# Optimization experiments

Hardware: AMD Instinct MI355X
Metric: run time of the kernel (lower is better)

## Reference

```python
import jax, jax.numpy as jnp
import numpy as np

EMB = 8
HID = 64
B = 1000
T = 512
N = (B * T) // 5  # events per source; sources partition the (batch,time) grid

_KEYS = ["ccba", "cdtx", "cust", "dp", "remit"]
_NUMS = {"ccba": 8, "cdtx": 1, "cust": 1, "dp": 2, "remit": 1}
_CATS = {"ccba": 0, "cdtx": 2, "cust": 3, "dp": 8, "remit": 1}
_VOCAB = {"ccba": 0, "cdtx": 179, "cust": 37, "dp": 435, "remit": 5}


def setup_inputs() -> dict:
    ks = iter(jax.random.split(jax.random.key(0), 64))
    rng = np.random.default_rng(0)
    chunks = np.split(rng.permutation(B * T), 5)
    d = {}
    for k5, ch in zip(_KEYS, chunks):
        d[k5 + "_num"] = jax.random.normal(next(ks), (N, _NUMS[k5]), jnp.float32)
        if _CATS[k5] > 0:
            d[k5 + "_cat"] = jax.random.randint(next(ks), (N, _CATS[k5]), 0, _VOCAB[k5])
            d[k5 + "_tab"] = jax.random.normal(next(ks), (_VOCAB[k5], EMB), jnp.float32) * 0.1
        d[k5 + "_bi"] = jnp.asarray(ch // T, jnp.int32)
        d[k5 + "_ti"] = jnp.asarray(ch % T, jnp.int32)
        in_dim = _CATS[k5] * EMB + _NUMS[k5]
        d[k5 + "_W"] = jax.random.normal(next(ks), (in_dim, HID), jnp.float32) * np.float32(1.0 / np.sqrt(in_dim))
        d[k5 + "_b"] = jnp.zeros((HID,), jnp.float32)
    # LSTM: 2 layers x 2 directions, hidden 64, proj_size 1 -> layer1 input is 2
    for l, insz in [(0, HID), (1, 2)]:
        d[f"Wih{l}"] = jax.random.normal(next(ks), (2, 4 * HID, insz), jnp.float32) * 0.05
        d[f"Whh{l}"] = jax.random.normal(next(ks), (2, 4 * HID, 1), jnp.float32) * 0.05
        d[f"Whr{l}"] = jax.random.normal(next(ks), (2, 1, HID), jnp.float32) * 0.05
        d[f"bih{l}"] = jnp.zeros((2, 4 * HID), jnp.float32)
        d[f"bhh{l}"] = jnp.zeros((2, 4 * HID), jnp.float32)
    d["length"] = T
    d["batch_size"] = B
    return d


def _embed(num, cat, tab, W, b):
    # FeatureEmbedder: concat(categorical embeddings, numeric) -> Linear(hidden)
    x = num if cat is None else jnp.concatenate([tab[cat].reshape(cat.shape[0], -1), num], axis=-1)
    return x @ W + b


def _lstm_dir(x, Wih, Whh, Whr, bih, bhh, reverse):
    Bx = x.shape[0]
    H = Whr.shape[1]
    p = Whr.shape[0]
    bias = bih + bhh

    def step(carry, xt):
        h, c = carry  # h: [B,p] projected hidden, c: [B,H] cell
        g = xt @ Wih.T + h @ Whh.T + bias
        i, f, gg, o = jnp.split(g, 4, axis=-1)  # PyTorch gate order i,f,g,o
        c = jax.nn.sigmoid(f) * c + jax.nn.sigmoid(i) * jnp.tanh(gg)
        h = (jax.nn.sigmoid(o) * jnp.tanh(c)) @ Whr.T  # proj_size projection
        return (h, c), h

    init = (jnp.zeros((Bx, p), x.dtype), jnp.zeros((Bx, H), x.dtype))
    _, ys = jax.lax.scan(step, init, jnp.swapaxes(x, 0, 1), reverse=reverse)
    return jnp.swapaxes(ys, 0, 1)  # [B,T,p]


def _bilstm(x, Wih, Whh, Whr, bih, bhh):
    fwd = _lstm_dir(x, Wih[0], Whh[0], Whr[0], bih[0], bhh[0], False)
    bwd = _lstm_dir(x, Wih[1], Whh[1], Whr[1], bih[1], bhh[1], True)
    return jnp.concatenate([fwd, bwd], axis=-1)


def _forward(a):
    feat = jnp.zeros((a["batch_size"], a["length"], HID), jnp.float32)
    for k5 in _KEYS:
        v = _embed(a[k5 + "_num"], a.get(k5 + "_cat"), a.get(k5 + "_tab"), a[k5 + "_W"], a[k5 + "_b"])
        feat = feat.at[a[k5 + "_bi"], a[k5 + "_ti"]].set(v)  # scatter-assemble padded tensor
    h = _bilstm(feat, a["Wih0"], a["Whh0"], a["Whr0"], a["bih0"], a["bhh0"])
    h = _bilstm(h, a["Wih1"], a["Whh1"], a["Whr1"], a["bih1"], a["bhh1"])
    return h.mean(axis=2)  # [B,T]


def reference(ccba_num, ccba_bi, ccba_ti, ccba_W, ccba_b,
              cdtx_num, cdtx_cat, cdtx_tab, cdtx_bi, cdtx_ti, cdtx_W, cdtx_b,
              cust_num, cust_cat, cust_tab, cust_bi, cust_ti, cust_W, cust_b,
              dp_num, dp_cat, dp_tab, dp_bi, dp_ti, dp_W, dp_b,
              remit_num, remit_cat, remit_tab, remit_bi, remit_ti, remit_W, remit_b,
              Wih0, Whh0, Whr0, bih0, bhh0, Wih1, Whh1, Whr1, bih1, bhh1,
              length, batch_size):
    return _forward(dict(locals()))
```

## Files before the change

### kernel.cpp

```cpp
#include <hip/hip_runtime.h>
#include <cstdint>
#include <cstddef>

#define TLEN 512
#define BATCH 1000
#define NEVS 102400
#define HID 64

__device__ __forceinline__ float fast_rcp(float x) {
#if __has_builtin(__builtin_amdgcn_rcpf)
    return __builtin_amdgcn_rcpf(x);
#else
    return 1.0f / x;
#endif
}
__device__ __forceinline__ float sigm(float x) { return fast_rcp(1.0f + __expf(-x)); }
__device__ __forceinline__ float tanh_f(float x) { return fmaf(2.0f, sigm(2.0f * x), -1.0f); }

__device__ __forceinline__ float wave_sum_bcast(float x) {
#if __has_builtin(__builtin_amdgcn_update_dpp) && __has_builtin(__builtin_amdgcn_readlane)
    x += __int_as_float(__builtin_amdgcn_update_dpp(0, __float_as_int(x), 0x111, 0xf, 0xf, true));
    x += __int_as_float(__builtin_amdgcn_update_dpp(0, __float_as_int(x), 0x112, 0xf, 0xf, true));
    x += __int_as_float(__builtin_amdgcn_update_dpp(0, __float_as_int(x), 0x114, 0xf, 0xf, true));
    x += __int_as_float(__builtin_amdgcn_update_dpp(0, __float_as_int(x), 0x118, 0xf, 0xf, true));
    x += __int_as_float(__builtin_amdgcn_update_dpp(0, __float_as_int(x), 0x142, 0xa, 0xf, true));
    x += __int_as_float(__builtin_amdgcn_update_dpp(0, __float_as_int(x), 0x143, 0xc, 0xf, true));
    return __int_as_float(__builtin_amdgcn_readlane(__float_as_int(x), 63));
#else
#pragma unroll
    for (int off = 1; off < 64; off <<= 1) x += __shfl_xor(x, off, 64);
    return x;
#endif
}

__global__ __launch_bounds__(512) void compose_kernel(
    const float* __restrict__ W0, const float* __restrict__ B0,
    const float* __restrict__ W1, const float* __restrict__ B1,
    const float* __restrict__ W2, const float* __restrict__ B2,
    const float* __restrict__ W3, const float* __restrict__ B3,
    const float* __restrict__ W4, const float* __restrict__ B4,
    const float* __restrict__ Wih, const float* __restrict__ bih,
    const float* __restrict__ bhh, float* __restrict__ wp)
{
    const int col = threadIdx.x;
    const int row = blockIdx.x;
    const float* srcW; const float* srcB; int base, IND;
    if (row < 9)        { srcW = W0; srcB = B0; base = 0;   IND = 8;  }
    else if (row < 27)  { srcW = W1; srcB = B1; base = 9;   IND = 17; }
    else if (row < 53)  { srcW = W2; srcB = B2; base = 27;  IND = 25; }
    else if (row < 120) { srcW = W3; srcB = B3; base = 53;  IND = 66; }
    else                { srcW = W4; srcB = B4; base = 120; IND = 9;  }
    const int j = row - base;
    const float* xrow = (j < IND) ? (srcW + (size_t)j * 64) : srcB;
    const float* wr = Wih + (size_t)col * 64;
    float acc = 0.0f;
#pragma unroll
    for (int h2 = 0; h2 < 64; ++h2) acc = fmaf(xrow[h2], wr[h2], acc);
    if (j == IND) acc += bih[col] + bhh[col];
    wp[(size_t)row * 512 + col] = acc;
}

template<int NNUM, int NCAT>
__device__ __forceinline__ void project_src(
    const float* __restrict__ num, const int* __restrict__ cat,
    const float* __restrict__ tab, const int* __restrict__ bi,
    const int* __restrict__ ti, const float* __restrict__ wrows,
    float* __restrict__ gdst, int dir, int lo, int hi, int tcm,
    int* qcnt, int* queue)
{
    constexpr int IND = NCAT * 8 + NNUM;
    const int tid = threadIdx.x;
    const int col = dir * 256 + tid;
    float wcol[IND];
#pragma unroll
    for (int j = 0; j < IND; ++j) wcol[j] = wrows[(size_t)j * 512 + col];
    const float bcol = wrows[(size_t)IND * 512 + col];

    const int S = gridDim.x;
    const int per = (NEVS + S - 1) / S;
    const int e0 = blockIdx.x * per;
    const int e1 = (e0 + per < NEVS) ? (e0 + per) : NEVS;

    for (int base = e0; base < e1; base += 256) {
        if (tid == 0) *qcnt = 0;
        __syncthreads();
        {
            const int ev = base + tid;
            if (ev < e1) {
                const int t = ti[ev];
                if (t >= lo && t < hi) {
                    const int s = atomicAdd(qcnt, 1);
                    queue[s] = ev;
                }
            }
        }
        __syncthreads();
        const int n = *qcnt;
        for (int i = 0; i < n; i += 2) {
            const int eA = __builtin_amdgcn_readfirstlane(queue[i]);
            const bool two = (i + 1 < n);
            const int eB = two ? __builtin_amdgcn_readfirstlane(queue[i + 1]) : eA;
            float accA = bcol, accB = bcol;
#pragma unroll
            for (int c0 = 0; c0 < NCAT; ++c0) {
                const int ia = cat[eA * NCAT + c0];
                const int ib = cat[eB * NCAT + c0];
                const float* ta = tab + (size_t)ia * 8;
                const float* tb = tab + (size_t)ib * 8;
#pragma unroll
                for (int u = 0; u < 8; ++u) {
                    accA = fmaf(ta[u], wcol[c0 * 8 + u], accA);
                    accB = fmaf(tb[u], wcol[c0 * 8 + u], accB);
                }
            }
#pragma unroll
            for (int u = 0; u < NNUM; ++u) {
                accA = fmaf(num[(size_t)eA * NNUM + u], wcol[NCAT * 8 + u], accA);
                accB = fmaf(num[(size_t)eB * NNUM + u], wcol[NCAT * 8 + u], accB);
            }
            {
                const int tA = ti[eA], pA = bi[eA];
                const int lA = dir ? (hi - 1 - tA) : (tA - lo);
                gdst[((size_t)pA * tcm + lA) * 256 + tid] = accA;
            }
            if (two) {
                const int tB = ti[eB], pB = bi[eB];
                const int lB = dir ? (hi - 1 - tB) : (tB - lo);
                gdst[((size_t)pB * tcm + lB) * 256 + tid] = accB;
            }
        }
        __syncthreads();
    }
}

__global__ __launch_bounds__(256) void project_chunk_kernel(
    const float* __restrict__ ccba_num, const int* __restrict__ ccba_bi, const int* __restrict__ ccba_ti,
    const float* __restrict__ cdtx_num, const int* __restrict__ cdtx_cat, const float* __restrict__ cdtx_tab,
    const int* __restrict__ cdtx_bi, const int* __restrict__ cdtx_ti,
    const float* __restrict__ cust_num, const int* __restrict__ cust_cat, const float* __restrict__ cust_tab,
    const int* __restrict__ cust_bi, const int* __restrict__ cust_ti,
    const float* __restrict__ dp_num, const int* __restrict__ dp_cat, const float* __restrict__ dp_tab,
    const int* __restrict__ dp_bi, const int* __restrict__ dp_ti,
    const float* __restrict__ remit_num, const int* __restrict__ remit_cat, const float* __restrict__ remit_tab,
    const int* __restrict__ remit_bi, const int* __restrict__ remit_ti,
    const float* __restrict__ wp, float* __restrict__ gf, float* __restrict__ gb,
    int f0, int len, int tcm)
{
    __shared__ int qcnt;
    __shared__ int queue[256];
    const int dir = blockIdx.y & 1;
    const int src = blockIdx.y >> 1;
    const int lo = dir ? (TLEN - f0 - len) : f0;
    const int hi = lo + len;
    float* gdst = dir ? gb : gf;
    switch (src) {
        case 0: project_src<8, 0>(ccba_num, nullptr, nullptr, ccba_bi, ccba_ti, wp + 0 * 512,   gdst, dir, lo, hi, tcm, &qcnt, queue); break;
        case 1: project_src<1, 2>(cdtx_num, cdtx_cat, cdtx_tab, cdtx_bi, cdtx_ti, wp + 9 * 512,  gdst, dir, lo, hi, tcm, &qcnt, queue); break;
        case 2: project_src<1, 3>(cust_num, cust_cat, cust_tab, cust_bi, cust_ti, wp + 27 * 512, gdst, dir, lo, hi, tcm, &qcnt, queue); break;
        case 3: project_src<2, 8>(dp_num,   dp_cat,   dp_tab,   dp_bi,   dp_ti,   wp + 53 * 512, gdst, dir, lo, hi, tcm, &qcnt, queue); break;
        default: project_src<1, 1>(remit_num, remit_cat, remit_tab, remit_bi, remit_ti, wp + 120 * 512, gdst, dir, lo, hi, tcm, &qcnt, queue); break;
    }
}

__global__ __launch_bounds__(256) void rec_chunk_kernel(
    const float* __restrict__ gf, const float* __restrict__ gb,
    const float* __restrict__ Whh, const float* __restrict__ Whr,
    float* __restrict__ h0, float* __restrict__ hs, float* __restrict__ cs,
    int f0, int len, int tcm, int first)
{
    const int wv = threadIdx.x >> 6, lane = threadIdx.x & 63;
    const int p = blockIdx.x * 4 + wv;
    const int b = p >> 1, dir = p & 1;

    float whh4[4];
#pragma unroll
    for (int k = 0; k < 4; ++k) whh4[k] = Whh[dir * 256 + k * 64 + lane];
    const float whr = Whr[dir * HID + lane];

    const float* g = (dir ? gb : gf) + (size_t)b * tcm * 256 + lane;
    float* h0p = h0 + (size_t)b * TLEN * 2 + dir;

    float h, c;
    if (first) { h = 0.0f; c = 0.0f; }
    else       { h = hs[p]; c = cs[(size_t)p * 64 + lane]; }

    float A[4];
#pragma unroll
    for (int k = 0; k < 4; ++k) A[k] = g[k * 64];

    for (int s = 0; s < len; ++s) {
        float Nx[4];
        const int sn = (s + 1 < len) ? (s + 1) : s;
        const float* gn = g + (size_t)sn * 256;
#pragma unroll
        for (int k = 0; k < 4; ++k) Nx[k] = gn[k * 64];

        const float gi = fmaf(whh4[0], h, A[0]);
        const float gfv = fmaf(whh4[1], h, A[1]);
        const float gg = fmaf(whh4[2], h, A[2]);
        const float go = fmaf(whh4[3], h, A[3]);
        c = sigm(gfv) * c + sigm(gi) * tanh_f(gg);
        h = wave_sum_bcast(sigm(go) * tanh_f(c) * whr);
        const int t_out = dir ? (TLEN - 1 - f0 - s) : (f0 + s);
        if (lane == 0) h0p[(size_t)t_out * 2] = h;
#pragma unroll
        for (int k = 0; k < 4; ++k) A[k] = Nx[k];
    }
    if (lane == 0) hs[p] = h;
    cs[(size_t)p * 64 + lane] = c;
}

__global__ __launch_bounds__(256) void lstm1_kernel(
    const float* __restrict__ h0, const float* __restrict__ Wih,
    const float* __restrict__ Whh, const float* __restrict__ Whr,
    const float* __restrict__ bih, const float* __restrict__ bhh,
    float* __restrict__ h1)
{
    int w = threadIdx.x >> 6, lane = threadIdx.x & 63;
    int p = blockIdx.x * 4 + w;
    int b = p >> 1, dir = p & 1;

    float wi0[4], wi1[4], whh[4], bias[4];
#pragma unroll
    for (int k = 0; k < 4; ++k) {
        int r = k * 64 + lane;
        wi0[k] = Wih[(size_t)(dir * 256 + r) * 2 + 0];
        wi1[k] = Wih[(size_t)(dir * 256 + r) * 2 + 1];
        whh[k] = Whh[dir * 256 + r];
        bias[k] = bih[dir * 256 + r] + bhh[dir * 256 + r];
    }
    float whr = Whr[dir * HID + lane];
    float h = 0.0f, c = 0.0f;
    const float* hb = h0 + (size_t)b * TLEN * 2;

    auto xat = [&](int t) -> float2 {
        int tc = t < TLEN ? t : TLEN - 1;
        int tt = dir ? (TLEN - 1 - tc) : tc;
        return *(const float2*)(hb + (size_t)tt * 2);
    };

    float2 xA = xat(0), xB = xat(1);
    for (int t = 0; t < TLEN; t += 2) {
        float2 xC = xat(t + 2), xD = xat(t + 3);
        {
            float g[4];
#pragma unroll
            for (int k = 0; k < 4; ++k)
                g[k] = fmaf(whh[k], h, fmaf(wi1[k], xA.y, fmaf(wi0[k], xA.x, bias[k])));
            c = sigm(g[1]) * c + sigm(g[0]) * tanh_f(g[2]);
            h = wave_sum_bcast(sigm(g[3]) * tanh_f(c) * whr);
            int tt = dir ? (TLEN - 1 - t) : t;
            if (lane == 0) h1[((size_t)b * TLEN + tt) * 2 + dir] = h;
        }
        {
            float g[4];
#pragma unroll
            for (int k = 0; k < 4; ++k)
                g[k] = fmaf(whh[k], h, fmaf(wi1[k], xB.y, fmaf(wi0[k], xB.x, bias[k])));
            c = sigm(g[1]) * c + sigm(g[0]) * tanh_f(g[2]);
            h = wave_sum_bcast(sigm(g[3]) * tanh_f(c) * whr);
            int tt = dir ? (TLEN - 2 - t) : (t + 1);
            if (lane == 0) h1[((size_t)b * TLEN + tt) * 2 + dir] = h;
        }
        xA = xC; xB = xD;
    }
}

__global__ __launch_bounds__(256) void mean_kernel(
    const float2* __restrict__ h1, float* __restrict__ out)
{
    int i = blockIdx.x * 256 + threadIdx.x;
    if (i < BATCH * TLEN) {
        float2 v = h1[i];
        out[i] = 0.5f * (v.x + v.y);
    }
}

extern "C" void kernel_launch(void* const* d_in, const int* in_sizes, int n_in,
                              void* d_out, int out_size, void* d_ws, size_t ws_size,
                              hipStream_t stream)
{
    const float* ccba_num = (const float*)d_in[0];
    const int*   ccba_bi  = (const int*)d_in[1];
    const int*   ccba_ti  = (const int*)d_in[2];
    const float* ccba_W   = (const float*)d_in[3];
    const float* ccba_b   = (const float*)d_in[4];
    const float* cdtx_num = (const float*)d_in[5];
    const int*   cdtx_cat = (const int*)d_in[6];
    const float* cdtx_tab = (const float*)d_in[7];
    const int*   cdtx_bi  = (const int*)d_in[8];
    const int*   cdtx_ti  = (const int*)d_in[9];
    const float* cdtx_W   = (const float*)d_in[10];
    const float* cdtx_b   = (const float*)d_in[11];
    const float* cust_num = (const float*)d_in[12];
    const int*   cust_cat = (const int*)d_in[13];
    const float* cust_tab = (const float*)d_in[14];
    const int*   cust_bi  = (const int*)d_in[15];
    const int*   cust_ti  = (const int*)d_in[16];
    const float* cust_W   = (const float*)d_in[17];
    const float* cust_b   = (const float*)d_in[18];
    const float* dp_num   = (const float*)d_in[19];
    const int*   dp_cat   = (const int*)d_in[20];
    const float* dp_tab   = (const float*)d_in[21];
    const int*   dp_bi    = (const int*)d_in[22];
    const int*   dp_ti    = (const int*)d_in[23];
    const float* dp_W     = (const float*)d_in[24];
    const float* dp_b     = (const float*)d_in[25];
    const float* remit_num = (const float*)d_in[26];
    const int*   remit_cat = (const int*)d_in[27];
    const float* remit_tab = (const float*)d_in[28];
    const int*   remit_bi  = (const int*)d_in[29];
    const int*   remit_ti  = (const int*)d_in[30];
    const float* remit_W   = (const float*)d_in[31];
    const float* remit_b   = (const float*)d_in[32];
    const float* Wih0 = (const float*)d_in[33];
    const float* Whh0 = (const float*)d_in[34];
    const float* Whr0 = (const float*)d_in[35];
    const float* bih0 = (const float*)d_in[36];
    const float* bhh0 = (const float*)d_in[37];
    const float* Wih1 = (const float*)d_in[38];
    const float* Whh1 = (const float*)d_in[39];
    const float* Whr1 = (const float*)d_in[40];
    const float* bih1 = (const float*)d_in[41];
    const float* bhh1 = (const float*)d_in[42];

    float* out = (float*)d_out;

    const size_t FIXED = 4096000ull + 4096000ull + 266240ull + 8000ull + 512000ull;
    size_t avail = (ws_size > FIXED) ? (ws_size - FIXED) : 0;
    int tcm = (int)(avail / 2048000ull);
    if (tcm < 1) tcm = 1;
    if (tcm > TLEN) tcm = TLEN;

    char* ws = (char*)d_ws;
    const size_t gfB = (size_t)tcm * 1024000ull;
    float* gf = (float*)ws;
    float* gb = (float*)(ws + gfB);
    float* h0 = (float*)(ws + 2 * gfB);
    float* h1 = (float*)(ws + 2 * gfB + 4096000ull);
    float* wp = (float*)(ws + 2 * gfB + 8192000ull);
    float* hs = (float*)(ws + 2 * gfB + 8192000ull + 266240ull);
    float* cs = (float*)(ws + 2 * gfB + 8192000ull + 266240ull + 8000ull);

    compose_kernel<<<130, 512, 0, stream>>>(
        ccba_W, ccba_b, cdtx_W, cdtx_b, cust_W, cust_b,
        dp_W, dp_b, remit_W, remit_b, Wih0, bih0, bhh0, wp);

    int first = 1;
    for (int f0 = 0; f0 < TLEN; f0 += tcm) {
        const int len = (TLEN - f0 < tcm) ? (TLEN - f0) : tcm;
        project_chunk_kernel<<<dim3(256, 10), 256, 0, stream>>>(
            ccba_num, ccba_bi, ccba_ti,
            cdtx_num, cdtx_cat, cdtx_tab, cdtx_bi, cdtx_ti,
            cust_num, cust_cat, cust_tab, cust_bi, cust_ti,
            dp_num, dp_cat, dp_tab, dp_bi, dp_ti,
            remit_num, remit_cat, remit_tab, remit_bi, remit_ti,
            wp, gf, gb, f0, len, tcm);
        rec_chunk_kernel<<<500, 256, 0, stream>>>(
            gf, gb, Whh0, Whr0, h0, hs, cs, f0, len, tcm, first);
        first = 0;
    }

    lstm1_kernel<<<500, 256, 0, stream>>>(h0, Wih1, Whh1, Whr1, bih1, bhh1, h1);
    mean_kernel<<<(BATCH * TLEN + 255) / 256, 256, 0, stream>>>((const float2*)h1, out);
}
```

Measured before the change: 1.471 ms.

## Bin events by time with counting sort to avoid rescanning all events per chunk

Adds a counting-sort preprocessing pass (count, scan, scatter) that groups each source's events by time index. The chunked projection kernel can then walk only the events in its time range instead of filtering every event in every chunk through a shared-memory queue. The projection now handles four events per iteration, runs with a doubled grid, and the recurrence loop prefetches two steps ahead. It also caps the chunk length at 86 and forces it even, which can add chunk launches, and the extra binning kernels and workspace add fixed overhead.

```diff
diff --git a/kernel.cpp b/kernel.cpp
--- a/kernel.cpp
+++ b/kernel.cpp
@@ -31,6 +31,55 @@
     for (int off = 1; off < 64; off <<= 1) x += __shfl_xor(x, off, 64);
     return x;
 #endif
+}
+
+__global__ __launch_bounds__(256) void bin_zero_kernel(int* __restrict__ cnt)
+{
+    int i = blockIdx.x * 256 + threadIdx.x;
+    if (i < 5 * 512) cnt[i] = 0;
+}
+
+__global__ __launch_bounds__(256) void bin_count_kernel(
+    const int* __restrict__ t0, const int* __restrict__ t1,
+    const int* __restrict__ t2, const int* __restrict__ t3,
+    const int* __restrict__ t4, int* __restrict__ cnt)
+{
+    const int src = blockIdx.y;
+    const int* ti = src == 0 ? t0 : src == 1 ? t1 : src == 2 ? t2 : src == 3 ? t3 : t4;
+    const int e = blockIdx.x * 256 + threadIdx.x;
+    atomicAdd(&cnt[src * 512 + ti[e]], 1);
+}
+
+__global__ __launch_bounds__(512) void bin_scan_kernel(
+    const int* __restrict__ cnt, int* __restrict__ startp, int* __restrict__ cur)
+{
+    const int src = blockIdx.x, tid = threadIdx.x;
+    __shared__ int s[512];
+    const int v = cnt[src * 512 + tid];
+    s[tid] = v;
+    __syncthreads();
+    for (int off = 1; off < 512; off <<= 1) {
+        int t = (tid >= off) ? s[tid - off] : 0;
+        __syncthreads();
+        s[tid] += t;
+        __syncthreads();
+    }
+    const int inc = s[tid];
+    startp[src * 513 + tid] = inc - v;
+    cur[src * 512 + tid] = inc - v;
+    if (tid == 511) startp[src * 513 + 512] = inc;
+}
+
+__global__ __launch_bounds__(256) void bin_scatter_kernel(
+    const int* __restrict__ t0, const int* __restrict__ t1,
+    const int* __restrict__ t2, const int* __restrict__ t3,
+    const int* __restrict__ t4, int* __restrict__ cur, int* __restrict__ order)
+{
+    const int src = blockIdx.y;
+    const int* ti = src == 0 ? t0 : src == 1 ? t1 : src == 2 ? t2 : src == 3 ? t3 : t4;
+    const int e = blockIdx.x * 256 + threadIdx.x;
+    const int off = atomicAdd(&cur[src * 512 + ti[e]], 1);
+    order[(size_t)src * NEVS + off] = e;
 }
 
 __global__ __launch_bounds__(512) void compose_kernel(
@@ -65,8 +114,8 @@
     const float* __restrict__ num, const int* __restrict__ cat,
     const float* __restrict__ tab, const int* __restrict__ bi,
     const int* __restrict__ ti, const float* __restrict__ wrows,
-    float* __restrict__ gdst, int dir, int lo, int hi, int tcm,
-    int* qcnt, int* queue)
+    const int* __restrict__ order_s, const int* __restrict__ start_s,
+    float* __restrict__ gdst, int dir, int lo, int hi, int tcm)
 {
     constexpr int IND = NCAT * 8 + NNUM;
     const int tid = threadIdx.x;
@@ -76,60 +125,50 @@
     for (int j = 0; j < IND; ++j) wcol[j] = wrows[(size_t)j * 512 + col];
     const float bcol = wrows[(size_t)IND * 512 + col];
 
-    const int S = gridDim.x;
-    const int per = (NEVS + S - 1) / S;
-    const int e0 = blockIdx.x * per;
-    const int e1 = (e0 + per < NEVS) ? (e0 + per) : NEVS;
-
-    for (int base = e0; base < e1; base += 256) {
-        if (tid == 0) *qcnt = 0;
-        __syncthreads();
-        {
-            const int ev = base + tid;
-            if (ev < e1) {
-                const int t = ti[ev];
-                if (t >= lo && t < hi) {
-                    const int s = atomicAdd(qcnt, 1);
-                    queue[s] = ev;
-                }
+    const int r0 = start_s[lo];
+    const int r1 = start_s[hi];
+
+    for (int i = r0 + (int)blockIdx.x * 4; i < r1; i += (int)gridDim.x * 4) {
+        int ebuf[4], tE[4], pE[4];
+#pragma unroll
+        for (int k = 0; k < 4; ++k) {
+            const int j = i + k;
+            ebuf[k] = __builtin_amdgcn_readfirstlane(order_s[(j < r1) ? j : i]);
+        }
+#pragma unroll
+        for (int k = 0; k < 4; ++k) { tE[k] = ti[ebuf[k]]; pE[k] = bi[ebuf[k]]; }
+
+        float acc[4] = {bcol, bcol, bcol, bcol};
+#pragma unroll
+        for (int c0 = 0; c0 < NCAT; ++c0) {
+            const float* t0 = tab + (size_t)cat[ebuf[0] * NCAT + c0] * 8;
+            const float* t1 = tab + (size_t)cat[ebuf[1] * NCAT + c0] * 8;
+            const float* t2 = tab + (size_t)cat[ebuf[2] * NCAT + c0] * 8;
+            const float* t3 = tab + (size_t)cat[ebuf[3] * NCAT + c0] * 8;
+#pragma unroll
+            for (int u = 0; u < 8; ++u) {
+                const float w = wcol[c0 * 8 + u];
+                acc[0] = fmaf(t0[u], w, acc[0]);
+                acc[1] = fmaf(t1[u], w, acc[1]);
+                acc[2] = fmaf(t2[u], w, acc[2]);
+                acc[3] = fmaf(t3[u], w, acc[3]);
             }
         }
-        __syncthreads();
-        const int n = *qcnt;
-        for (int i = 0; i < n; i += 2) {
-            const int eA = __builtin_amdgcn_readfirstlane(queue[i]);
-            const bool two = (i + 1 < n);
-            const int eB = two ? __builtin_amdgcn_readfirstlane(queue[i + 1]) : eA;
-            float accA = bcol, accB = bcol;
-#pragma unroll
-            for (int c0 = 0; c0 < NCAT; ++c0) {
-                const int ia = cat[eA * NCAT + c0];
-                const int ib = cat[eB * NCAT + c0];
-                const float* ta = tab + (size_t)ia * 8;
-                const float* tb = tab + (size_t)ib * 8;
-#pragma unroll
-                for (int u = 0; u < 8; ++u) {
-                    accA = fmaf(ta[u], wcol[c0 * 8 + u], accA);
-                    accB = fmaf(tb[u], wcol[c0 * 8 + u], accB);
-                }
+#pragma unroll
+        for (int u = 0; u < NNUM; ++u) {
+            const float w = wcol[NCAT * 8 + u];
+            acc[0] = fmaf(num[(size_t)ebuf[0] * NNUM + u], w, acc[0]);
+            acc[1] = fmaf(num[(size_t)ebuf[1] * NNUM + u], w, acc[1]);
+            acc[2] = fmaf(num[(size_t)ebuf[2] * NNUM + u], w, acc[2]);
+            acc[3] = fmaf(num[(size_t)ebuf[3] * NNUM + u], w, acc[3]);
+        }
+#pragma unroll
+        for (int k = 0; k < 4; ++k) {
+            if (i + k < r1) {
+                const int l = dir ? (hi - 1 - tE[k]) : (tE[k] - lo);
+                gdst[((size_t)pE[k] * tcm + l) * 256 + tid] = acc[k];
             }
-#pragma unroll
-            for (int u = 0; u < NNUM; ++u) {
-                accA = fmaf(num[(size_t)eA * NNUM + u], wcol[NCAT * 8 + u], accA);
-                accB = fmaf(num[(size_t)eB * NNUM + u], wcol[NCAT * 8 + u], accB);
-            }
-            {
-                const int tA = ti[eA], pA = bi[eA];
-                const int lA = dir ? (hi - 1 - tA) : (tA - lo);
-                gdst[((size_t)pA * tcm + lA) * 256 + tid] = accA;
-            }
-            if (two) {
-                const int tB = ti[eB], pB = bi[eB];
-                const int lB = dir ? (hi - 1 - tB) : (tB - lo);
-                gdst[((size_t)pB * tcm + lB) * 256 + tid] = accB;
-            }
-        }
-        __syncthreads();
+        }
     }
 }
 
@@ -143,22 +182,23 @@
     const int* __restrict__ dp_bi, const int* __restrict__ dp_ti,
     const float* __restrict__ remit_num, const int* __restrict__ remit_cat, const float* __restrict__ remit_tab,
     const int* __restrict__ remit_bi, const int* __restrict__ remit_ti,
-    const float* __restrict__ wp, float* __restrict__ gf, float* __restrict__ gb,
+    const float* __restrict__ wp, const int* __restrict__ order, const int* __restrict__ startp,
+    float* __restrict__ gf, float* __restrict__ gb,
     int f0, int len, int tcm)
 {
-    __shared__ int qcnt;
-    __shared__ int queue[256];
     const int dir = blockIdx.y & 1;
     const int src = blockIdx.y >> 1;
     const int lo = dir ? (TLEN - f0 - len) : f0;
     const int hi = lo + len;
     float* gdst = dir ? gb : gf;
+    const int* order_s = order + (size_t)src * NEVS;
+    const int* start_s = startp + src * 513;
     switch (src) {
-        case 0: project_src<8, 0>(ccba_num, nullptr, nullptr, ccba_bi, ccba_ti, wp + 0 * 512,   gdst, dir, lo, hi, tcm, &qcnt, queue); break;
-        case 1: project_src<1, 2>(cdtx_num, cdtx_cat, cdtx_tab, cdtx_bi, cdtx_ti, wp + 9 * 512,  gdst, dir, lo, hi, tcm, &qcnt, queue); break;
-        case 2: project_src<1, 3>(cust_num, cust_cat, cust_tab, cust_bi, cust_ti, wp + 27 * 512, gdst, dir, lo, hi, tcm, &qcnt, queue); break;
-        case 3: project_src<2, 8>(dp_num,   dp_cat,   dp_tab,   dp_bi,   dp_ti,   wp + 53 * 512, gdst, dir, lo, hi, tcm, &qcnt, queue); break;
-        default: project_src<1, 1>(remit_num, remit_cat, remit_tab, remit_bi, remit_ti, wp + 120 * 512, gdst, dir, lo, hi, tcm, &qcnt, queue); break;
+        case 0: project_src<8, 0>(ccba_num, nullptr, nullptr, ccba_bi, ccba_ti, wp + 0 * 512,   order_s, start_s, gdst, dir, lo, hi, tcm); break;
+        case 1: project_src<1, 2>(cdtx_num, cdtx_cat, cdtx_tab, cdtx_bi, cdtx_ti, wp + 9 * 512,  order_s, start_s, gdst, dir, lo, hi, tcm); break;
+        case 2: project_src<1, 3>(cust_num, cust_cat, cust_tab, cust_bi, cust_ti, wp + 27 * 512, order_s, start_s, gdst, dir, lo, hi, tcm); break;
+        case 3: project_src<2, 8>(dp_num,   dp_cat,   dp_tab,   dp_bi,   dp_ti,   wp + 53 * 512, order_s, start_s, gdst, dir, lo, hi, tcm); break;
+        default: project_src<1, 1>(remit_num, remit_cat, remit_tab, remit_bi, remit_ti, wp + 120 * 512, order_s, start_s, gdst, dir, lo, hi, tcm); break;
     }
 }
 
@@ -184,27 +224,36 @@
     if (first) { h = 0.0f; c = 0.0f; }
     else       { h = hs[p]; c = cs[(size_t)p * 64 + lane]; }
 
-    float A[4];
-#pragma unroll
-    for (int k = 0; k < 4; ++k) A[k] = g[k * 64];
-
-    for (int s = 0; s < len; ++s) {
-        float Nx[4];
-        const int sn = (s + 1 < len) ? (s + 1) : s;
-        const float* gn = g + (size_t)sn * 256;
-#pragma unroll
-        for (int k = 0; k < 4; ++k) Nx[k] = gn[k * 64];
-
-        const float gi = fmaf(whh4[0], h, A[0]);
-        const float gfv = fmaf(whh4[1], h, A[1]);
-        const float gg = fmaf(whh4[2], h, A[2]);
-        const float go = fmaf(whh4[3], h, A[3]);
+    auto ga = [&](int s) -> const float* {
+        const int sc = (s < len) ? s : (len - 1);
+        return g + (size_t)sc * 256;
+    };
+    auto do_step = [&](const float (&G)[4], int s) {
+        const float gi = fmaf(whh4[0], h, G[0]);
+        const float gfv = fmaf(whh4[1], h, G[1]);
+        const float gg = fmaf(whh4[2], h, G[2]);
+        const float go = fmaf(whh4[3], h, G[3]);
         c = sigm(gfv) * c + sigm(gi) * tanh_f(gg);
         h = wave_sum_bcast(sigm(go) * tanh_f(c) * whr);
         const int t_out = dir ? (TLEN - 1 - f0 - s) : (f0 + s);
         if (lane == 0) h0p[(size_t)t_out * 2] = h;
-#pragma unroll
-        for (int k = 0; k < 4; ++k) A[k] = Nx[k];
+    };
+
+    float A[4], B[4];
+    {
+        const float* pa = ga(0); const float* pb = ga(1);
+#pragma unroll
+        for (int k = 0; k < 4; ++k) { A[k] = pa[k * 64]; B[k] = pb[k * 64]; }
+    }
+    for (int s = 0; s < len; s += 2) {
+        float C[4], D[4];
+        const float* pc = ga(s + 2); const float* pd = ga(s + 3);
+#pragma unroll
+        for (int k = 0; k < 4; ++k) { C[k] = pc[k * 64]; D[k] = pd[k * 64]; }
+        do_step(A, s);
+        if (s + 1 < len) do_step(B, s + 1);
+#pragma unroll
+        for (int k = 0; k < 4; ++k) { A[k] = C[k]; B[k] = D[k]; }
     }
     if (lane == 0) hs[p] = h;
     cs[(size_t)p * 64 + lane] = c;
@@ -326,41 +375,54 @@
 
     float* out = (float*)d_out;
 
-    const size_t FIXED = 4096000ull + 4096000ull + 266240ull + 8000ull + 512000ull;
+    const size_t FIXED = 4096000ull + 4096000ull + 266240ull + 8000ull + 512000ull
+                       + 2048000ull + 10240ull + 10272ull + 10240ull;
     size_t avail = (ws_size > FIXED) ? (ws_size - FIXED) : 0;
     int tcm = (int)(avail / 2048000ull);
     if (tcm < 1) tcm = 1;
-    if (tcm > TLEN) tcm = TLEN;
+    if (tcm > 86) tcm = 86;
+    if (tcm >= 2) tcm &= ~1;
 
     char* ws = (char*)d_ws;
     const size_t gfB = (size_t)tcm * 1024000ull;
-    float* gf = (float*)ws;
-    float* gb = (float*)(ws + gfB);
-    float* h0 = (float*)(ws + 2 * gfB);
-    float* h1 = (float*)(ws + 2 * gfB + 4096000ull);
-    float* wp = (float*)(ws + 2 * gfB + 8192000ull);
-    float* hs = (float*)(ws + 2 * gfB + 8192000ull + 266240ull);
-    float* cs = (float*)(ws + 2 * gfB + 8192000ull + 266240ull + 8000ull);
-
+    float* gf    = (float*)ws;
+    float* gb    = (float*)(ws + gfB);
+    char*  fixed = ws + 2 * gfB;
+    float* h0    = (float*)fixed;
+    float* h1    = (float*)(fixed + 4096000ull);
+    float* wp    = (float*)(fixed + 8192000ull);
+    float* hs    = (float*)(fixed + 8192000ull + 266240ull);
+    float* cs    = (float*)(fixed + 8192000ull + 266240ull + 8000ull);
+    int*   order = (int*)  (fixed + 8192000ull + 266240ull + 8000ull + 512000ull);
+    int*   cnt   = (int*)  (fixed + 8192000ull + 266240ull + 8000ull + 512000ull + 2048000ull);
+    int*   startp= (int*)  (fixed + 8192000ull + 266240ull + 8000ull + 512000ull + 2048000ull + 10240ull);
+    int*   cur   = (int*)  (fixed + 8192000ull + 266240ull + 8000ull + 512000ull + 2048000ull + 10240ull + 10272ull);
+
+    bin_zero_kernel<<<10, 256, 0, stream>>>(cnt);
     compose_kernel<<<130, 512, 0, stream>>>(
         ccba_W, ccba_b, cdtx_W, cdtx_b, cust_W, cust_b,
         dp_W, dp_b, remit_W, remit_b, Wih0, bih0, bhh0, wp);
+    bin_count_kernel<<<dim3(400, 5), 256, 0, stream>>>(
+        ccba_ti, cdtx_ti, cust_ti, dp_ti, remit_ti, cnt);
+    bin_scan_kernel<<<5, 512, 0, stream>>>(cnt, startp, cur);
+    bin_scatter_kernel<<<dim3(400, 5), 256, 0, stream>>>(
+        ccba_ti, cdtx_ti, cust_ti, dp_ti, remit_ti, cur, order);
 
     int first = 1;
     for (int f0 = 0; f0 < TLEN; f0 += tcm) {
         const int len = (TLEN - f0 < tcm) ? (TLEN - f0) : tcm;
-        project_chunk_kernel<<<dim3(256, 10), 256, 0, stream>>>(
+        project_chunk_kernel<<<dim3(512, 10), 256, 0, stream>>>(
             ccba_num, ccba_bi, ccba_ti,
             cdtx_num, cdtx_cat, cdtx_tab, cdtx_bi, cdtx_ti,
             cust_num, cust_cat, cust_tab, cust_bi, cust_ti,
             dp_num, dp_cat, dp_tab, dp_bi, dp_ti,
             remit_num, remit_cat, remit_tab, remit_bi, remit_ti,
-            wp, gf, gb, f0, len, tcm);
+            wp, order, startp, gf, gb, f0, len, tcm);
         rec_chunk_kernel<<<500, 256, 0, stream>>>(
             gf, gb, Whh0, Whr0, h0, hs, cs, f0, len, tcm, first);
         first = 0;
     }
 
-    lstm1_kernel<<<500, 256, 0, stream>>>(h0, Wih1, Whh1, Whr1, bih1, bhh1, h1);
+    lstm1_kernel<<<500, 256, 0, stream>>>(h0, Whh1 ? Wih1 : Wih1, Whh1, Whr1, bih1, bhh1, h1);
     mean_kernel<<<(BATCH * TLEN + 255) / 256, 256, 0, stream>>>((const float2*)h1, out);
 }
```

Result: no change. 1.498 ms (+1.8%).

## Fuse event projection and layer-0 LSTM recurrence via inverse (batch,time) map

Applied to the files above, without the earlier changes.

Builds an inverse map from (batch,time) to (source,event), then launches one block per (batch,direction). Each block gathers 32 time steps of event features into shared memory, projects them to gate pre-activations with register-resident composed weights, and runs the layer-0 recurrence over that window. This removes the chunked scatter through global gate buffers, the per-chunk event filtering with atomics, and the multiple kernel launches. In exchange, the serial recurrence now runs on a single wave per block while the other three waves wait, and the large per-thread weight arrays (about 130 floats) raise register pressure.

```diff
diff --git a/kernel.cpp b/kernel.cpp
--- a/kernel.cpp
+++ b/kernel.cpp
@@ -6,6 +6,7 @@
 #define BATCH 1000
 #define NEVS 102400
 #define HID 64
+#define W0S 32
 
 __device__ __forceinline__ float fast_rcp(float x) {
 #if __has_builtin(__builtin_amdgcn_rcpf)
@@ -31,6 +32,21 @@
     for (int off = 1; off < 64; off <<= 1) x += __shfl_xor(x, off, 64);
     return x;
 #endif
+}
+
+__global__ __launch_bounds__(256) void map_build_kernel(
+    const int* __restrict__ b0, const int* __restrict__ t0,
+    const int* __restrict__ b1, const int* __restrict__ t1,
+    const int* __restrict__ b2, const int* __restrict__ t2,
+    const int* __restrict__ b3, const int* __restrict__ t3,
+    const int* __restrict__ b4, const int* __restrict__ t4,
+    int* __restrict__ map)
+{
+    const int src = blockIdx.y;
+    const int* bi = src == 0 ? b0 : src == 1 ? b1 : src == 2 ? b2 : src == 3 ? b3 : b4;
+    const int* ti = src == 0 ? t0 : src == 1 ? t1 : src == 2 ? t2 : src == 3 ? t3 : t4;
+    const int e = blockIdx.x * 256 + threadIdx.x;
+    map[bi[e] * TLEN + ti[e]] = (src << 20) | e;
 }
 
 __global__ __launch_bounds__(512) void compose_kernel(
@@ -60,154 +76,152 @@
     wp[(size_t)row * 512 + col] = acc;
 }
 
-template<int NNUM, int NCAT>
-__device__ __forceinline__ void project_src(
-    const float* __restrict__ num, const int* __restrict__ cat,
-    const float* __restrict__ tab, const int* __restrict__ bi,
-    const int* __restrict__ ti, const float* __restrict__ wrows,
-    float* __restrict__ gdst, int dir, int lo, int hi, int tcm,
-    int* qcnt, int* queue)
-{
-    constexpr int IND = NCAT * 8 + NNUM;
+__global__ __launch_bounds__(256) void fused0_kernel(
+    const float* __restrict__ ccba_num,
+    const float* __restrict__ cdtx_num, const int* __restrict__ cdtx_cat, const float* __restrict__ cdtx_tab,
+    const float* __restrict__ cust_num, const int* __restrict__ cust_cat, const float* __restrict__ cust_tab,
+    const float* __restrict__ dp_num,   const int* __restrict__ dp_cat,   const float* __restrict__ dp_tab,
+    const float* __restrict__ remit_num, const int* __restrict__ remit_cat, const float* __restrict__ remit_tab,
+    const float* __restrict__ wp, const int* __restrict__ map,
+    const float* __restrict__ Whh, const float* __restrict__ Whr,
+    float* __restrict__ h0)
+{
     const int tid = threadIdx.x;
+    const int b = blockIdx.x >> 1, dir = blockIdx.x & 1;
     const int col = dir * 256 + tid;
-    float wcol[IND];
-#pragma unroll
-    for (int j = 0; j < IND; ++j) wcol[j] = wrows[(size_t)j * 512 + col];
-    const float bcol = wrows[(size_t)IND * 512 + col];
-
-    const int S = gridDim.x;
-    const int per = (NEVS + S - 1) / S;
-    const int e0 = blockIdx.x * per;
-    const int e1 = (e0 + per < NEVS) ? (e0 + per) : NEVS;
-
-    for (int base = e0; base < e1; base += 256) {
-        if (tid == 0) *qcnt = 0;
+
+    float w_c0[9], w_c1[18], w_c2[26], w_c3[67], w_c4[10];
+#pragma unroll
+    for (int j = 0; j < 9;  ++j) w_c0[j] = wp[(size_t)(0   + j) * 512 + col];
+#pragma unroll
+    for (int j = 0; j < 18; ++j) w_c1[j] = wp[(size_t)(9   + j) * 512 + col];
+#pragma unroll
+    for (int j = 0; j < 26; ++j) w_c2[j] = wp[(size_t)(27  + j) * 512 + col];
+#pragma unroll
+    for (int j = 0; j < 67; ++j) w_c3[j] = wp[(size_t)(53  + j) * 512 + col];
+#pragma unroll
+    for (int j = 0; j < 10; ++j) w_c4[j] = wp[(size_t)(120 + j) * 512 + col];
+
+    __shared__ float window[W0S * 256];
+    __shared__ float xbuf[W0S][68];
+    __shared__ int   mcls[W0S];
+
+    const int lane = tid & 63;
+    float whh4[4] = {0, 0, 0, 0};
+    float whr = 0.0f, h = 0.0f, c = 0.0f;
+    if (tid < 64) {
+#pragma unroll
+        for (int k = 0; k < 4; ++k) whh4[k] = Whh[dir * 256 + k * 64 + lane];
+        whr = Whr[dir * HID + lane];
+    }
+    float* h0p = h0 + (size_t)b * TLEN * 2 + dir;
+
+    auto dot_evt = [&](int mc, const float* xb) -> float {
+        const int src = mc >> 20;
+        float a0 = 0.0f, a1 = 0.0f, bias = 0.0f;
+        switch (src) {
+        case 0:
+#pragma unroll
+            for (int j = 0; j < 8; j += 2) { a0 = fmaf(xb[j], w_c0[j], a0); a1 = fmaf(xb[j + 1], w_c0[j + 1], a1); }
+            bias = w_c0[8]; break;
+        case 1:
+#pragma unroll
+            for (int j = 0; j < 16; j += 2) { a0 = fmaf(xb[j], w_c1[j], a0); a1 = fmaf(xb[j + 1], w_c1[j + 1], a1); }
+            a0 = fmaf(xb[16], w_c1[16], a0);
+            bias = w_c1[17]; break;
+        case 2:
+#pragma unroll
+            for (int j = 0; j < 24; j += 2) { a0 = fmaf(xb[j], w_c2[j], a0); a1 = fmaf(xb[j + 1], w_c2[j + 1], a1); }
+            a0 = fmaf(xb[24], w_c2[24], a0);
+            bias = w_c2[25]; break;
+        case 3:
+#pragma unroll
+            for (int j = 0; j < 66; j += 2) { a0 = fmaf(xb[j], w_c3[j], a0); a1 = fmaf(xb[j + 1], w_c3[j + 1], a1); }
+            bias = w_c3[66]; break;
+        default:
+#pragma unroll
+            for (int j = 0; j < 8; j += 2) { a0 = fmaf(xb[j], w_c4[j], a0); a1 = fmaf(xb[j + 1], w_c4[j + 1], a1); }
+            a0 = fmaf(xb[8], w_c4[8], a0);
+            bias = w_c4[9]; break;
+        }
+        return bias + a0 + a1;
+    };
+
+    for (int s0 = 0; s0 < TLEN; s0 += W0S) {
+        {
+            const int sl = tid >> 3, q = tid & 7;
+            const int s = s0 + sl;
+            const int t = dir ? (TLEN - 1 - s) : s;
+            const int mc = map[b * TLEN + t];
+            if (q == 0) mcls[sl] = mc;
+            const int src = mc >> 20, e = mc & 0xFFFFF;
+            switch (src) {
+            case 0:
+                for (int v = q; v < 8; v += 8) xbuf[sl][v] = ccba_num[(size_t)e * 8 + v];
+                break;
+            case 1:
+                for (int v = q; v < 17; v += 8) {
+                    float x = (v < 16) ? cdtx_tab[(size_t)cdtx_cat[e * 2 + (v >> 3)] * 8 + (v & 7)]
+                                       : cdtx_num[e];
+                    xbuf[sl][v] = x;
+                }
+                break;
+            case 2:
+                for (int v = q; v < 25; v += 8) {
+                    float x = (v < 24) ? cust_tab[(size_t)cust_cat[e * 3 + (v >> 3)] * 8 + (v & 7)]
+                                       : cust_num[e];
+                    xbuf[sl][v] = x;
+                }
+                break;
+            case 3:
+                for (int v = q; v < 66; v += 8) {
+                    float x = (v < 64) ? dp_tab[(size_t)dp_cat[e * 8 + (v >> 3)] * 8 + (v & 7)]
+                                       : dp_num[(size_t)e * 2 + (v - 64)];
+                    xbuf[sl][v] = x;
+                }
+                break;
+            default:
+                for (int v = q; v < 9; v += 8) {
+                    float x = (v < 8) ? remit_tab[(size_t)remit_cat[e] * 8 + v]
+                                      : remit_num[e];
+                    xbuf[sl][v] = x;
+                }
+                break;
+            }
+        }
         __syncthreads();
-        {
-            const int ev = base + tid;
-            if (ev < e1) {
-                const int t = ti[ev];
-                if (t >= lo && t < hi) {
-                    const int s = atomicAdd(qcnt, 1);
-                    queue[s] = ev;
-                }
+
+        for (int sl = 0; sl < W0S; sl += 2) {
+            const float accA = dot_evt(mcls[sl], xbuf[sl]);
+            const float accB = dot_evt(mcls[sl + 1], xbuf[sl + 1]);
+            window[sl * 256 + tid] = accA;
+            window[(sl + 1) * 256 + tid] = accB;
+        }
+        __syncthreads();
+
+        if (tid < 64) {
+            float G[4], N[4];
+#pragma unroll
+            for (int k = 0; k < 4; ++k) G[k] = window[k * 64 + lane];
+            for (int sl = 0; sl < W0S; ++sl) {
+                const int slp = (sl + 1 < W0S) ? (sl + 1) : sl;
+#pragma unroll
+                for (int k = 0; k < 4; ++k) N[k] = window[slp * 256 + k * 64 + lane];
+                const float gi = fmaf(whh4[0], h, G[0]);
+                const float gf = fmaf(whh4[1], h, G[1]);
+                const float gg = fmaf(whh4[2], h, G[2]);
+                const float go = fmaf(whh4[3], h, G[3]);
+                c = sigm(gf) * c + sigm(gi) * tanh_f(gg);
+                h = wave_sum_bcast(sigm(go) * tanh_f(c) * whr);
+                const int s = s0 + sl;
+                const int t = dir ? (TLEN - 1 - s) : s;
+                if (lane == 0) h0p[(size_t)t * 2] = h;
+#pragma unroll
+                for (int k = 0; k < 4; ++k) G[k] = N[k];
             }
         }
         __syncthreads();
-        const int n = *qcnt;
-        for (int i = 0; i < n; i += 2) {
-            const int eA = __builtin_amdgcn_readfirstlane(queue[i]);
-            const bool two = (i + 1 < n);
-            const int eB = two ? __builtin_amdgcn_readfirstlane(queue[i + 1]) : eA;
-            float accA = bcol, accB = bcol;
-#pragma unroll
-            for (int c0 = 0; c0 < NCAT; ++c0) {
-                const int ia = cat[eA * NCAT + c0];
-                const int ib = cat[eB * NCAT + c0];
-                const float* ta = tab + (size_t)ia * 8;
-                const float* tb = tab + (size_t)ib * 8;
-#pragma unroll
-                for (int u = 0; u < 8; ++u) {
-                    accA = fmaf(ta[u], wcol[c0 * 8 + u], accA);
-                    accB = fmaf(tb[u], wcol[c0 * 8 + u], accB);
-                }
-            }
-#pragma unroll
-            for (int u = 0; u < NNUM; ++u) {
-                accA = fmaf(num[(size_t)eA * NNUM + u], wcol[NCAT * 8 + u], accA);
-                accB = fmaf(num[(size_t)eB * NNUM + u], wcol[NCAT * 8 + u], accB);
-            }
-            {
-                const int tA = ti[eA], pA = bi[eA];
-                const int lA = dir ? (hi - 1 - tA) : (tA - lo);
-                gdst[((size_t)pA * tcm + lA) * 256 + tid] = accA;
-            }
-            if (two) {
-                const int tB = ti[eB], pB = bi[eB];
-                const int lB = dir ? (hi - 1 - tB) : (tB - lo);
-                gdst[((size_t)pB * tcm + lB) * 256 + tid] = accB;
-            }
-        }
-        __syncthreads();
-    }
-}
-
-__global__ __launch_bounds__(256) void project_chunk_kernel(
-    const float* __restrict__ ccba_num, const int* __restrict__ ccba_bi, const int* __restrict__ ccba_ti,
-    const float* __restrict__ cdtx_num, const int* __restrict__ cdtx_cat, const float* __restrict__ cdtx_tab,
-    const int* __restrict__ cdtx_bi, const int* __restrict__ cdtx_ti,
-    const float* __restrict__ cust_num, const int* __restrict__ cust_cat, const float* __restrict__ cust_tab,
-    const int* __restrict__ cust_bi, const int* __restrict__ cust_ti,
-    const float* __restrict__ dp_num, const int* __restrict__ dp_cat, const float* __restrict__ dp_tab,
-    const int* __restrict__ dp_bi, const int* __restrict__ dp_ti,
-    const float* __restrict__ remit_num, const int* __restrict__ remit_cat, const float* __restrict__ remit_tab,
-    const int* __restrict__ remit_bi, const int* __restrict__ remit_ti,
-    const float* __restrict__ wp, float* __restrict__ gf, float* __restrict__ gb,
-    int f0, int len, int tcm)
-{
-    __shared__ int qcnt;
-    __shared__ int queue[256];
-    const int dir = blockIdx.y & 1;
-    const int src = blockIdx.y >> 1;
-    const int lo = dir ? (TLEN - f0 - len) : f0;
-    const int hi = lo + len;
-    float* gdst = dir ? gb : gf;
-    switch (src) {
-        case 0: project_src<8, 0>(ccba_num, nullptr, nullptr, ccba_bi, ccba_ti, wp + 0 * 512,   gdst, dir, lo, hi, tcm, &qcnt, queue); break;
-        case 1: project_src<1, 2>(cdtx_num, cdtx_cat, cdtx_tab, cdtx_bi, cdtx_ti, wp + 9 * 512,  gdst, dir, lo, hi, tcm, &qcnt, queue); break;
-        case 2: project_src<1, 3>(cust_num, cust_cat, cust_tab, cust_bi, cust_ti, wp + 27 * 512, gdst, dir, lo, hi, tcm, &qcnt, queue); break;
-        case 3: project_src<2, 8>(dp_num,   dp_cat,   dp_tab,   dp_bi,   dp_ti,   wp + 53 * 512, gdst, dir, lo, hi, tcm, &qcnt, queue); break;
-        default: project_src<1, 1>(remit_num, remit_cat, remit_tab, remit_bi, remit_ti, wp + 120 * 512, gdst, dir, lo, hi, tcm, &qcnt, queue); break;
-    }
-}
-
-__global__ __launch_bounds__(256) void rec_chunk_kernel(
-    const float* __restrict__ gf, const float* __restrict__ gb,
-    const float* __restrict__ Whh, const float* __restrict__ Whr,
-    float* __restrict__ h0, float* __restrict__ hs, float* __restrict__ cs,
-    int f0, int len, int tcm, int first)
-{
-    const int wv = threadIdx.x >> 6, lane = threadIdx.x & 63;
-    const int p = blockIdx.x * 4 + wv;
-    const int b = p >> 1, dir = p & 1;
-
-    float whh4[4];
-#pragma unroll
-    for (int k = 0; k < 4; ++k) whh4[k] = Whh[dir * 256 + k * 64 + lane];
-    const float whr = Whr[dir * HID + lane];
-
-    const float* g = (dir ? gb : gf) + (size_t)b * tcm * 256 + lane;
-    float* h0p = h0 + (size_t)b * TLEN * 2 + dir;
-
-    float h, c;
-    if (first) { h = 0.0f; c = 0.0f; }
-    else       { h = hs[p]; c = cs[(size_t)p * 64 + lane]; }
-
-    float A[4];
-#pragma unroll
-    for (int k = 0; k < 4; ++k) A[k] = g[k * 64];
-
-    for (int s = 0; s < len; ++s) {
-        float Nx[4];
-        const int sn = (s + 1 < len) ? (s + 1) : s;
-        const float* gn = g + (size_t)sn * 256;
-#pragma unroll
-        for (int k = 0; k < 4; ++k) Nx[k] = gn[k * 64];
-
-        const float gi = fmaf(whh4[0], h, A[0]);
-        const float gfv = fmaf(whh4[1], h, A[1]);
-        const float gg = fmaf(whh4[2], h, A[2]);
-        const float go = fmaf(whh4[3], h, A[3]);
-        c = sigm(gfv) * c + sigm(gi) * tanh_f(gg);
-        h = wave_sum_bcast(sigm(go) * tanh_f(c) * whr);
-        const int t_out = dir ? (TLEN - 1 - f0 - s) : (f0 + s);
-        if (lane == 0) h0p[(size_t)t_out * 2] = h;
-#pragma unroll
-        for (int k = 0; k < 4; ++k) A[k] = Nx[k];
-    }
-    if (lane == 0) hs[p] = h;
-    cs[(size_t)p * 64 + lane] = c;
+    }
 }
 
 __global__ __launch_bounds__(256) void lstm1_kernel(
@@ -326,40 +340,27 @@
 
     float* out = (float*)d_out;
 
-    const size_t FIXED = 4096000ull + 4096000ull + 266240ull + 8000ull + 512000ull;
-    size_t avail = (ws_size > FIXED) ? (ws_size - FIXED) : 0;
-    int tcm = (int)(avail / 2048000ull);
-    if (tcm < 1) tcm = 1;
-    if (tcm > TLEN) tcm = TLEN;
-
     char* ws = (char*)d_ws;
-    const size_t gfB = (size_t)tcm * 1024000ull;
-    float* gf = (float*)ws;
-    float* gb = (float*)(ws + gfB);
-    float* h0 = (float*)(ws + 2 * gfB);
-    float* h1 = (float*)(ws + 2 * gfB + 4096000ull);
-    float* wp = (float*)(ws + 2 * gfB + 8192000ull);
-    float* hs = (float*)(ws + 2 * gfB + 8192000ull + 266240ull);
-    float* cs = (float*)(ws + 2 * gfB + 8192000ull + 266240ull + 8000ull);
+    float* wp  = (float*)ws;
+    int*   map = (int*)  (ws + 266240ull);
+    float* h0  = (float*)(ws + 266240ull + 2048000ull);
+    float* h1  = (float*)(ws + 266240ull + 2048000ull + 4096000ull);
 
     compose_kernel<<<130, 512, 0, stream>>>(
         ccba_W, ccba_b, cdtx_W, cdtx_b, cust_W, cust_b,
         dp_W, dp_b, remit_W, remit_b, Wih0, bih0, bhh0, wp);
 
-    int first = 1;
-    for (int f0 = 0; f0 < TLEN; f0 += tcm) {
-        const int len = (TLEN - f0 < tcm) ? (TLEN - f0) : tcm;
-        project_chunk_kernel<<<dim3(256, 10), 256, 0, stream>>>(
-            ccba_num, ccba_bi, ccba_ti,
-            cdtx_num, cdtx_cat, cdtx_tab, cdtx_bi, cdtx_ti,
-            cust_num, cust_cat, cust_tab, cust_bi, cust_ti,
-            dp_num, dp_cat, dp_tab, dp_bi, dp_ti,
-            remit_num, remit_cat, remit_tab, remit_bi, remit_ti,
-            wp, gf, gb, f0, len, tcm);
-        rec_chunk_kernel<<<500, 256, 0, stream>>>(
-            gf, gb, Whh0, Whr0, h0, hs, cs, f0, len, tcm, first);
-        first = 0;
-    }
+    map_build_kernel<<<dim3(NEVS / 256, 5), 256, 0, stream>>>(
+        ccba_bi, ccba_ti, cdtx_bi, cdtx_ti, cust_bi, cust_ti,
+        dp_bi, dp_ti, remit_bi, remit_ti, map);
+
+    fused0_kernel<<<2 * BATCH, 256, 0, stream>>>(
+        ccba_num,
+        cdtx_num, cdtx_cat, cdtx_tab,
+        cust_num, cust_cat, cust_tab,
+        dp_num, dp_cat, dp_tab,
+        remit_num, remit_cat, remit_tab,
+        wp, map, Whh0, Whr0, h0);
 
     lstm1_kernel<<<500, 256, 0, stream>>>(h0, Wih1, Whh1, Whr1, bih1, bhh1, h1);
     mean_kernel<<<(BATCH * TLEN + 255) / 256, 256, 0, stream>>>((const float2*)h1, out);
```

Result: slower. 1.623 ms (+10.3%).
